# Performance work log

Hardware: AMD Instinct MI355X
Metric: run time of the kernel (lower is better)

Reference implementation:

```python
import jax, jax.numpy as jnp
import numpy as np

N = 10000        # nodes
E = 160000       # edges (avg degree 16)
MUL = 16         # multiplicity of each irrep in node features: '16x0e + 16x1o'
DIM_IN = 4 * MUL # 16 scalars + 16 vectors(3) = 64
DIM_SH = 4       # '1x0e + 1x1o' spherical harmonics
EMB = 18         # 2*4 (type embeds) + 10 (distance embed)
HID = 256
WNUM = 4 * MUL * MUL  # 4 tensor-product paths, 16x16 weights each


def setup_inputs() -> dict:
    key = jax.random.key(0)
    ks = jax.random.split(key, 8)
    node_features = jax.random.normal(ks[0], (N, DIM_IN), jnp.float32)
    edge_src = jax.random.randint(ks[1], (E,), 0, N, dtype=jnp.int32)
    edge_dst = jax.random.randint(ks[2], (E,), 0, N, dtype=jnp.int32)
    edge_attr = jax.random.normal(ks[3], (E, DIM_SH), jnp.float32)
    edge_embedding = jax.random.normal(ks[4], (E, EMB), jnp.float32)
    W1 = jax.random.normal(ks[5], (EMB, HID), jnp.float32) / np.sqrt(EMB)
    b1 = jnp.zeros((HID,), jnp.float32)
    W2 = jax.random.normal(ks[6], (HID, WNUM), jnp.float32) / np.sqrt(HID)
    b2 = jnp.zeros((WNUM,), jnp.float32)
    return dict(node_features=node_features, edge_attr=edge_attr,
                edge_embedding=edge_embedding, W1=W1, b1=b1, W2=W2, b2=b2,
                edge_src=edge_src, edge_dst=edge_dst)


def reference(node_features, edge_attr, edge_embedding, W1, b1, W2, b2, edge_src, edge_dst):
    # ---- edge MLP generates per-edge tensor-product weights ----
    h = jax.nn.silu(edge_embedding @ W1 + b1)          # [E, HID]
    w = (h @ W2 + b2).reshape(E, 4, MUL, MUL)          # [E, 4, 16, 16]
    w_ss, w_vv, w_sv, w_vs = w[:, 0], w[:, 1], w[:, 2], w[:, 3]

    # ---- gather source node features, split into irreps ----
    x = node_features[edge_src]                        # [E, 64]
    s = x[:, :MUL]                                     # [E, 16]   16x0e
    v = x[:, MUL:].reshape(E, MUL, 3)                  # [E, 16, 3] 16x1o
    y0 = edge_attr[:, 0]                               # [E]       1x0e sh
    y1 = edge_attr[:, 1:4]                             # [E, 3]    1x1o sh

    # ---- weighted Clebsch-Gordan tensor product (lmax=1 paths) ----
    inv_sqrt3 = np.float32(1.0 / np.sqrt(3.0))         # w3j(1,1,0), w3j(0,1,1), w3j(1,0,1)
    c_s = np.float32(np.sqrt(1.0 / (2 * MUL)))         # path norm: 2 paths, fan_in MUL each, out dim 1
    c_v = np.float32(np.sqrt(3.0 / (2 * MUL)))         # path norm: 2 paths, fan_in MUL each, out dim 3
    # 0e x 0e -> 0e  and  1o x 1o -> 0e
    out_s = c_s * (jnp.einsum('eij,e,ei->ej', w_ss, y0, s)
                   + inv_sqrt3 * jnp.einsum('eij,ea,eia->ej', w_vv, y1, v))   # [E, 16]
    # 0e x 1o -> 1o  and  1o x 0e -> 1o
    out_v = (c_v * inv_sqrt3) * (jnp.einsum('eij,ei,ea->eja', w_sv, s, y1)
                                 + jnp.einsum('eij,eia,e->eja', w_vs, v, y0))  # [E, 16, 3]

    edge_features = jnp.concatenate([out_s, out_v.reshape(E, 3 * MUL)], axis=1)  # [E, 64]

    # ---- scatter-reduce to destination nodes, normalized by sqrt(avg degree) ----
    num_neighbors = E / float(N)
    out = jax.ops.segment_sum(edge_features, edge_dst, num_segments=N)
    return out / np.float32(np.sqrt(num_neighbors))
```

## Files before the change

kernel.cpp:

```cpp
#include <hip/hip_runtime.h>
#include <math.h>


typedef __attribute__((ext_vector_type(8))) short s8v;
typedef __attribute__((ext_vector_type(4))) float f4v;
typedef unsigned short ushort_t;
typedef unsigned int uint_t;

#define NTHR 256
#define TE 64

__device__ __forceinline__ ushort_t f2bf(float x) {
    uint_t u = __float_as_uint(x);
    u += 0x7fffu + ((u >> 16) & 1u);
    return (ushort_t)(u >> 16);
}
__device__ __forceinline__ float bf2f(ushort_t v) {
    return __uint_as_float((uint_t)v << 16);
}

__global__ void prep_kernel(const float* __restrict__ W2, ushort_t* __restrict__ W2bf,
                            const int* __restrict__ edst, int* __restrict__ counts, int E) {
    if (blockIdx.x < 256) {
        int idx = blockIdx.x * 256 + threadIdx.x;
        int n  = idx & 1023;
        int k4 = (idx >> 10) << 2;
        uint_t lo = (uint_t)f2bf(W2[(size_t)(k4 + 0) * 1024 + n]) |
                    ((uint_t)f2bf(W2[(size_t)(k4 + 1) * 1024 + n]) << 16);
        uint_t hi = (uint_t)f2bf(W2[(size_t)(k4 + 2) * 1024 + n]) |
                    ((uint_t)f2bf(W2[(size_t)(k4 + 3) * 1024 + n]) << 16);
        ((uint2*)W2bf)[(n * 256 + k4) >> 2] = make_uint2(lo, hi);
    } else {
        int i = (blockIdx.x - 256) * 256 + threadIdx.x;
        if (i < E) atomicAdd(&counts[edst[i]], 1);
    }
}

__global__ __launch_bounds__(1024)
void scan_kernel(const int* __restrict__ counts, int* __restrict__ offsets, int N) {
    __shared__ int sdata[1024];
    const int t = threadIdx.x;
    const int C = (N + 1023) / 1024;
    const int lo = t * C;
    const int hi = min(lo + C, N);
    int sum = 0;
    for (int i = lo; i < hi; ++i) sum += counts[i];
    sdata[t] = sum;
    __syncthreads();
    for (int s = 1; s < 1024; s <<= 1) {
        int v = (t >= s) ? sdata[t - s] : 0;
        __syncthreads();
        sdata[t] += v;
        __syncthreads();
    }
    int run = sdata[t] - sum;
    for (int i = lo; i < hi; ++i) { offsets[i] = run; run += counts[i]; }
    if (t == 1023) offsets[N] = run;
}

__global__ __launch_bounds__(256)
void gather_kernel(const ushort_t* __restrict__ F,
                   const int* __restrict__ offsets,
                   const int* __restrict__ elist,
                   float* __restrict__ out, int N) {
    const int lane = threadIdx.x & 63;
    const int node = (blockIdx.x * 256 + threadIdx.x) >> 6;
    if (node >= N) return;
    const int base = offsets[node];
    const int end  = offsets[node + 1];
    float acc = 0.f;
    for (int j0 = base; j0 < end; j0 += 64) {
        const int rem = min(64, end - j0);
        int myeid = (lane < rem) ? elist[j0 + lane] : 0;
        int j = 0;
        for (; j + 4 <= rem; j += 4) {
            const int a0 = __shfl(myeid, j    );
            const int a1 = __shfl(myeid, j + 1);
            const int a2 = __shfl(myeid, j + 2);
            const int a3 = __shfl(myeid, j + 3);
            const float r0 = bf2f(F[(size_t)a0 * 64 + lane]);
            const float r1 = bf2f(F[(size_t)a1 * 64 + lane]);
            const float r2 = bf2f(F[(size_t)a2 * 64 + lane]);
            const float r3 = bf2f(F[(size_t)a3 * 64 + lane]);
            acc += (r0 + r1) + (r2 + r3);
        }
        for (; j < rem; ++j) {
            const int a = __shfl(myeid, j);
            acc += bf2f(F[(size_t)a * 64 + lane]);
        }
    }
    out[(size_t)node * 64 + lane] = acc;
}

#define LDB(sl_, g_, kk_) do { \
    const size_t o0 = (size_t)(slab * 256 + (g_) * 32) * 256 + (kk_) * 32; \
    sb0[sl_] = *(const s8v*)(Bl + o0); \
    sb1[sl_] = *(const s8v*)(Bl + o0 + 16 * 256); \
} while (0)

__global__ __launch_bounds__(NTHR, 2)
void nequip_mfma(const float* __restrict__ nodef,
                 const float* __restrict__ eattr,
                 const float* __restrict__ eemb,
                 const float* __restrict__ W1,
                 const float* __restrict__ b1,
                 const ushort_t* __restrict__ W2bf,
                 const float* __restrict__ b2,
                 const int* __restrict__ esrc,
                 const int* __restrict__ edst,
                 const int* __restrict__ offs,
                 int* __restrict__ cursor,
                 int* __restrict__ elist,
                 ushort_t* __restrict__ F,
                 int E, float CC)
{
    __shared__ __align__(16) ushort_t sAu[TE * 256];
    __shared__ __align__(16) float sB2[1024];
    __shared__ __align__(16) float sEmb[TE * 18];
    __shared__ __align__(16) float sCss[16 * 64];
    __shared__ __align__(16) float sCvv[16 * 64];
    __shared__ __align__(16) float sCsv[16 * 64];
    __shared__ __align__(16) float sCvs[48 * 64];
    __shared__ __align__(16) float sAttrT[4 * 64];
    __shared__ __align__(16) float resSS[64 * 16];
    __shared__ __align__(16) float resSV[64 * 16];

    const int t  = threadIdx.x;
    const int e0 = blockIdx.x * TE;

    ((float4*)sB2)[t] = ((const float4*)b2)[t];
    for (int idx = t; idx < TE * 18; idx += NTHR) {
        size_t g = (size_t)e0 * 18 + idx;
        sEmb[idx] = (g < (size_t)E * 18) ? eemb[g] : 0.f;
    }
    if (t < TE) {
        int ge = e0 + t;
        float4 a = make_float4(0.f, 0.f, 0.f, 0.f);
        if (ge < E) {
            a = *(const float4*)(eattr + (size_t)ge * 4);
            const int d = edst[ge];
            const int pos = offs[d] + atomicAdd(&cursor[d], 1);
            elist[pos] = ge;
        }
        sAttrT[0 * 64 + t] = a.x; sAttrT[1 * 64 + t] = a.y;
        sAttrT[2 * 64 + t] = a.z; sAttrT[3 * 64 + t] = a.w;
    }
    {
        const int e = t >> 2, iq = t & 3;
        const int ge = e0 + e;
        const bool ok = ge < E;
        float y0 = 0.f, y1x = 0.f, y1y = 0.f, y1z = 0.f;
        int src = 0;
        if (ok) {
            float4 a = *(const float4*)(eattr + (size_t)ge * 4);
            y0 = a.x; y1x = a.y; y1y = a.z; y1z = a.w;
            src = esrc[ge];
        }
        const float* xp = nodef + (size_t)src * 64;
        float4 z = make_float4(0.f, 0.f, 0.f, 0.f);
        float4 sv = ok ? *(const float4*)(xp + iq * 4) : z;
        float4 v0 = ok ? *(const float4*)(xp + 16 + iq * 12) : z;
        float4 v1 = ok ? *(const float4*)(xp + 16 + iq * 12 + 4) : z;
        float4 v2 = ok ? *(const float4*)(xp + 16 + iq * 12 + 8) : z;
        const float K3 = CC * 0.57735026918962576f;
        float sarr[4] = { sv.x, sv.y, sv.z, sv.w };
        float varr[12] = { v0.x, v0.y, v0.z, v0.w, v1.x, v1.y, v1.z, v1.w,
                           v2.x, v2.y, v2.z, v2.w };
        #pragma unroll
        for (int j = 0; j < 4; ++j) {
            const int i = iq * 4 + j;
            const float s  = sarr[j];
            const float vx = varr[j * 3 + 0], vy = varr[j * 3 + 1], vz = varr[j * 3 + 2];
            sCss[i * 64 + e] = CC * y0 * s;
            sCvv[i * 64 + e] = K3 * (y1x * vx + y1y * vy + y1z * vz);
            sCsv[i * 64 + e] = CC * s;
            sCvs[(i * 3 + 0) * 64 + e] = CC * y0 * vx;
            sCvs[(i * 3 + 1) * 64 + e] = CC * y0 * vy;
            sCvs[(i * 3 + 2) * 64 + e] = CC * y0 * vz;
        }
    }
    __syncthreads();

    {
        const int p = t & 127;
        const int ehalf = t >> 7;
        const int n0 = 2 * p;
        float w1a[18], w1b[18];
        #pragma unroll
        for (int m = 0; m < 18; ++m) {
            float2 wv = *(const float2*)(W1 + m * 256 + n0);
            w1a[m] = wv.x; w1b[m] = wv.y;
        }
        const float2 bv = *(const float2*)(b1 + n0);
        const int kk = p >> 4;
        const int lhi = 16 * ((p >> 2) & 3);
        const int wsub = p & 3;
        uint_t* sA32 = (uint_t*)sAu;
        for (int er = 0; er < 32; ++er) {
            const int e = ehalf * 32 + er;
            float a0 = bv.x, a1 = bv.y;
            const float* ep = sEmb + e * 18;
            #pragma unroll
            for (int m = 0; m < 18; ++m) {
                const float em = ep[m];
                a0 = fmaf(em, w1a[m], a0);
                a1 = fmaf(em, w1b[m], a1);
            }
            a0 = a0 / (1.f + __expf(-a0));
            a1 = a1 / (1.f + __expf(-a1));
            const uint_t pk = (uint_t)f2bf(a0) | ((uint_t)f2bf(a1) << 16);
            const int lane_sw = ((e & 15) + lhi) ^ kk;
            sA32[(((e >> 4) * 8 + kk) * 64 + lane_sw) * 4 + wsub] = pk;
        }
    }
    __syncthreads();

    const int lane = t & 63;
    const int slab = t >> 6;
    const int jj   = lane & 15;
    const int q4   = lane >> 4;

    const ushort_t* Bl = W2bf + (size_t)jj * 256 + q4 * 8;

    float pS[4][4] = {{0.f}};
    float pV[3][4][4] = {{{0.f}}};

    if (slab < 3) {
        const float* C = (slab == 0) ? sCss : (slab == 1) ? sCvv : sCsv;
        s8v sb0[4], sb1[4];
        LDB(0, 0, 0); LDB(1, 0, 1); LDB(2, 0, 2); LDB(3, 0, 3);
        #pragma unroll 1
        for (int g = 0; g < 8; ++g) {
            const int nb0 = slab * 256 + g * 32;
            const int nb1 = nb0 + 16;
            f4v accA[4], accB[4];
            {
                const float bz0 = sB2[nb0 + jj];
                const float bz1 = sB2[nb1 + jj];
                #pragma unroll
                for (int mt = 0; mt < 4; ++mt) {
                    f4v zA; zA[0] = bz0; zA[1] = bz0; zA[2] = bz0; zA[3] = bz0;
                    f4v zB; zB[0] = bz1; zB[1] = bz1; zB[2] = bz1; zB[3] = bz1;
                    accA[mt] = zA; accB[mt] = zB;
                }
            }
            #pragma unroll
            for (int kk = 0; kk < 8; ++kk) {
                const s8v b0 = sb0[kk & 3];
                const s8v b1 = sb1[kk & 3];
                #pragma unroll
                for (int mt = 0; mt < 4; ++mt) {
                    const s8v a = *(const s8v*)(sAu + ((mt * 8 + kk) * 64 + (lane ^ kk)) * 8);
                    accA[mt] = __builtin_amdgcn_mfma_f32_16x16x32_bf16(a, b0, accA[mt], 0, 0, 0);
                    accB[mt] = __builtin_amdgcn_mfma_f32_16x16x32_bf16(a, b1, accB[mt], 0, 0, 0);
                }
                if (kk < 4) { LDB(kk, g, kk + 4); }
                else        { LDB(kk - 4, (g + 1) & 7, kk - 4); }
            }
            const int i0 = 2 * g, i1 = 2 * g + 1;
            #pragma unroll
            for (int mt = 0; mt < 4; ++mt) {
                const int ebase = mt * 16 + q4 * 4;
                const float4 c0 = *(const float4*)(C + i0 * 64 + ebase);
                const float4 c1 = *(const float4*)(C + i1 * 64 + ebase);
                pS[mt][0] += c0.x * accA[mt][0] + c1.x * accB[mt][0];
                pS[mt][1] += c0.y * accA[mt][1] + c1.y * accB[mt][1];
                pS[mt][2] += c0.z * accA[mt][2] + c1.z * accB[mt][2];
                pS[mt][3] += c0.w * accA[mt][3] + c1.w * accB[mt][3];
            }
        }
        if (slab == 0) {
            #pragma unroll
            for (int mt = 0; mt < 4; ++mt)
                #pragma unroll
                for (int q = 0; q < 4; ++q)
                    resSS[(mt * 16 + q4 * 4 + q) * 16 + jj] = pS[mt][q];
        } else if (slab == 2) {
            #pragma unroll
            for (int mt = 0; mt < 4; ++mt)
                #pragma unroll
                for (int q = 0; q < 4; ++q)
                    resSV[(mt * 16 + q4 * 4 + q) * 16 + jj] = pS[mt][q];
        }
    } else {
        s8v sb0[4], sb1[4];
        #pragma unroll
        for (int half = 0; half < 2; ++half) {
            LDB(0, 0, 0); LDB(1, 0, 1); LDB(2, 0, 2); LDB(3, 0, 3);
            #pragma unroll 1
            for (int g = 0; g < 8; ++g) {
                const int i0 = 2 * g, i1 = 2 * g + 1;
                const int nb0 = 3 * 256 + g * 32;
                const int nb1 = nb0 + 16;
                f4v acc0[2], acc1[2];
                {
                    const float bz0 = sB2[nb0 + jj];
                    const float bz1 = sB2[nb1 + jj];
                    #pragma unroll
                    for (int mt = 0; mt < 2; ++mt) {
                        f4v z0; z0[0] = bz0; z0[1] = bz0; z0[2] = bz0; z0[3] = bz0;
                        f4v z1; z1[0] = bz1; z1[1] = bz1; z1[2] = bz1; z1[3] = bz1;
                        acc0[mt] = z0; acc1[mt] = z1;
                    }
                }
                #pragma unroll
                for (int kk = 0; kk < 8; ++kk) {
                    const s8v b0 = sb0[kk & 3];
                    const s8v b1 = sb1[kk & 3];
                    #pragma unroll
                    for (int mt = 0; mt < 2; ++mt) {
                        const int mtg = half * 2 + mt;
                        const s8v a = *(const s8v*)(sAu + ((mtg * 8 + kk) * 64 + (lane ^ kk)) * 8);
                        acc0[mt] = __builtin_amdgcn_mfma_f32_16x16x32_bf16(a, b0, acc0[mt], 0, 0, 0);
                        acc1[mt] = __builtin_amdgcn_mfma_f32_16x16x32_bf16(a, b1, acc1[mt], 0, 0, 0);
                    }
                    if (kk < 4) { LDB(kk, g, kk + 4); }
                    else        { LDB(kk - 4, (g + 1) & 7, kk - 4); }
                }
                #pragma unroll
                for (int mt = 0; mt < 2; ++mt) {
                    const int mtg = half * 2 + mt;
                    const int ebase = mtg * 16 + q4 * 4;
                    #pragma unroll
                    for (int a = 0; a < 3; ++a) {
                        const float4 c0 = *(const float4*)(sCvs + (i0 * 3 + a) * 64 + ebase);
                        const float4 c1 = *(const float4*)(sCvs + (i1 * 3 + a) * 64 + ebase);
                        pV[a][mtg][0] += c0.x * acc0[mt][0] + c1.x * acc1[mt][0];
                        pV[a][mtg][1] += c0.y * acc0[mt][1] + c1.y * acc1[mt][1];
                        pV[a][mtg][2] += c0.z * acc0[mt][2] + c1.z * acc1[mt][2];
                        pV[a][mtg][3] += c0.w * acc0[mt][3] + c1.w * acc1[mt][3];
                    }
                }
            }
        }
    }
    __syncthreads();

    if (slab == 1) {
        #pragma unroll
        for (int mt = 0; mt < 4; ++mt) {
            #pragma unroll
            for (int q = 0; q < 4; ++q) {
                const int e = mt * 16 + q4 * 4 + q;
                const int ge = e0 + e;
                if (ge < E) F[(size_t)ge * 64 + jj] = f2bf(resSS[e * 16 + jj] + pS[mt][q]);
            }
        }
    } else if (slab == 3) {
        #pragma unroll
        for (int mt = 0; mt < 4; ++mt) {
            #pragma unroll
            for (int q = 0; q < 4; ++q) {
                const int e = mt * 16 + q4 * 4 + q;
                const int ge = e0 + e;
                const float sv = resSV[e * 16 + jj];
                if (ge < E) {
                    #pragma unroll
                    for (int a = 0; a < 3; ++a)
                        F[(size_t)ge * 64 + 16 + jj * 3 + a] =
                            f2bf(fmaf(sAttrT[(1 + a) * 64 + e], sv, pV[a][mt][q]));
                }
            }
        }
    }
}

extern "C" void kernel_launch(void* const* d_in, const int* in_sizes, int n_in,
                              void* d_out, int out_size, void* d_ws, size_t ws_size,
                              hipStream_t stream)
{
    const float* node_features = (const float*)d_in[0];
    const float* edge_attr     = (const float*)d_in[1];
    const float* edge_emb      = (const float*)d_in[2];
    const float* W1            = (const float*)d_in[3];
    const float* b1            = (const float*)d_in[4];
    const float* W2            = (const float*)d_in[5];
    const float* b2            = (const float*)d_in[6];
    const int*   edge_src      = (const int*)d_in[7];
    const int*   edge_dst      = (const int*)d_in[8];
    float*       out           = (float*)d_out;

    const int E = in_sizes[7];
    const int N = out_size / 64;
    const float num_neigh = (float)E / (float)N;
    const float CC = 0.17677669529663689f / sqrtf(num_neigh);

    char* ws = (char*)d_ws;
    size_t off = 0;
    auto alloc = [&](size_t bytes) { char* p = ws + off; off = (off + bytes + 255) & ~(size_t)255; return p; };
    ushort_t* W2bf   = (ushort_t*)alloc((size_t)1024 * 256 * 2);
    int*      counts = (int*)alloc((size_t)2 * N * 4);
    int*      cursor = counts + N;
    int*      offs   = (int*)alloc((size_t)(N + 1) * 4);
    int*      elist  = (int*)alloc((size_t)E * 4);
    ushort_t* F      = (ushort_t*)alloc((size_t)E * 64 * 2);
    (void)ws_size;

    hipMemsetAsync(counts, 0, (size_t)2 * N * 4, stream);

    const int histBlocks = (E + 255) / 256;
    prep_kernel<<<256 + histBlocks, 256, 0, stream>>>(W2, W2bf, edge_dst, counts, E);
    scan_kernel<<<1, 1024, 0, stream>>>(counts, offs, N);

    const int blocks = (E + TE - 1) / TE;
    nequip_mfma<<<blocks, NTHR, 0, stream>>>(
        node_features, edge_attr, edge_emb, W1, b1, W2bf, b2,
        edge_src, edge_dst, offs, cursor, elist, F, E, CC);

    gather_kernel<<<(N + 3) / 4, 256, 0, stream>>>(F, offs, elist, out, N);
}
```

Measured before the change: 343.7 us.

## Move first edge-MLP layer into prep kernel and stage hidden activations via global

The first MLP layer (embedding times W1 plus SiLU, packed to bf16 in the swizzled MFMA layout) moves out of the main MFMA kernel into extra blocks of the prep kernel. Its results go to a global buffer, and the main kernel copies its 32KB tile straight into shared memory. The aim is to shorten the main kernel and run this work alongside the W2 conversion and histogram. The cost is writing and reading E*256 bf16 values (about 82MB) through global memory.

```diff
diff --git a/kernel.cpp b/kernel.cpp
--- a/kernel.cpp
+++ b/kernel.cpp
@@ -20,9 +20,14 @@
 }
 
 __global__ void prep_kernel(const float* __restrict__ W2, ushort_t* __restrict__ W2bf,
-                            const int* __restrict__ edst, int* __restrict__ counts, int E) {
+                            const int* __restrict__ edst, int* __restrict__ counts,
+                            const float* __restrict__ eemb, const float* __restrict__ W1,
+                            const float* __restrict__ b1, ushort_t* __restrict__ hG,
+                            int E, int histBlocks) {
+    __shared__ float sEmb[TE * 18];
+    const int t = threadIdx.x;
     if (blockIdx.x < 256) {
-        int idx = blockIdx.x * 256 + threadIdx.x;
+        int idx = blockIdx.x * 256 + t;
         int n  = idx & 1023;
         int k4 = (idx >> 10) << 2;
         uint_t lo = (uint_t)f2bf(W2[(size_t)(k4 + 0) * 1024 + n]) |
@@ -30,9 +35,47 @@
         uint_t hi = (uint_t)f2bf(W2[(size_t)(k4 + 2) * 1024 + n]) |
                     ((uint_t)f2bf(W2[(size_t)(k4 + 3) * 1024 + n]) << 16);
         ((uint2*)W2bf)[(n * 256 + k4) >> 2] = make_uint2(lo, hi);
+    } else if ((int)blockIdx.x < 256 + histBlocks) {
+        int i = (blockIdx.x - 256) * 256 + t;
+        if (i < E) atomicAdd(&counts[edst[i]], 1);
     } else {
-        int i = (blockIdx.x - 256) * 256 + threadIdx.x;
-        if (i < E) atomicAdd(&counts[edst[i]], 1);
+        const int tile = blockIdx.x - 256 - histBlocks;
+        const int e0 = tile * TE;
+        for (int idx = t; idx < TE * 18; idx += NTHR) {
+            size_t g = (size_t)e0 * 18 + idx;
+            sEmb[idx] = (g < (size_t)E * 18) ? eemb[g] : 0.f;
+        }
+        __syncthreads();
+        const int p = t & 127;
+        const int ehalf = t >> 7;
+        const int n0 = 2 * p;
+        float w1a[18], w1b[18];
+        #pragma unroll
+        for (int m = 0; m < 18; ++m) {
+            float2 wv = *(const float2*)(W1 + m * 256 + n0);
+            w1a[m] = wv.x; w1b[m] = wv.y;
+        }
+        const float2 bv = *(const float2*)(b1 + n0);
+        const int kk = p >> 4;
+        const int lhi = 16 * ((p >> 2) & 3);
+        const int wsub = p & 3;
+        uint_t* hT = (uint_t*)hG + (size_t)tile * 8192;
+        for (int er = 0; er < 32; ++er) {
+            const int e = ehalf * 32 + er;
+            float a0 = bv.x, a1 = bv.y;
+            const float* ep = sEmb + e * 18;
+            #pragma unroll
+            for (int m = 0; m < 18; ++m) {
+                const float em = ep[m];
+                a0 = fmaf(em, w1a[m], a0);
+                a1 = fmaf(em, w1b[m], a1);
+            }
+            a0 = a0 / (1.f + __expf(-a0));
+            a1 = a1 / (1.f + __expf(-a1));
+            const uint_t pk = (uint_t)f2bf(a0) | ((uint_t)f2bf(a1) << 16);
+            const int lane_sw = ((e & 15) + lhi) ^ kk;
+            hT[(((e >> 4) * 8 + kk) * 64 + lane_sw) * 4 + wsub] = pk;
+        }
     }
 }
 
@@ -101,9 +144,7 @@
 __global__ __launch_bounds__(NTHR, 2)
 void nequip_mfma(const float* __restrict__ nodef,
                  const float* __restrict__ eattr,
-                 const float* __restrict__ eemb,
-                 const float* __restrict__ W1,
-                 const float* __restrict__ b1,
+                 const ushort_t* __restrict__ hG,
                  const ushort_t* __restrict__ W2bf,
                  const float* __restrict__ b2,
                  const int* __restrict__ esrc,
@@ -116,7 +157,6 @@
 {
     __shared__ __align__(16) ushort_t sAu[TE * 256];
     __shared__ __align__(16) float sB2[1024];
-    __shared__ __align__(16) float sEmb[TE * 18];
     __shared__ __align__(16) float sCss[16 * 64];
     __shared__ __align__(16) float sCvv[16 * 64];
     __shared__ __align__(16) float sCsv[16 * 64];
@@ -128,11 +168,13 @@
     const int t  = threadIdx.x;
     const int e0 = blockIdx.x * TE;
 
+    {
+        const uint4* hsrc = (const uint4*)(hG + (size_t)blockIdx.x * 16384);
+        uint4* sdst = (uint4*)sAu;
+        #pragma unroll
+        for (int r = 0; r < 8; ++r) sdst[r * 256 + t] = hsrc[r * 256 + t];
+    }
     ((float4*)sB2)[t] = ((const float4*)b2)[t];
-    for (int idx = t; idx < TE * 18; idx += NTHR) {
-        size_t g = (size_t)e0 * 18 + idx;
-        sEmb[idx] = (g < (size_t)E * 18) ? eemb[g] : 0.f;
-    }
     if (t < TE) {
         int ge = e0 + t;
         float4 a = make_float4(0.f, 0.f, 0.f, 0.f);
@@ -177,40 +219,6 @@
             sCvs[(i * 3 + 0) * 64 + e] = CC * y0 * vx;
             sCvs[(i * 3 + 1) * 64 + e] = CC * y0 * vy;
             sCvs[(i * 3 + 2) * 64 + e] = CC * y0 * vz;
-        }
-    }
-    __syncthreads();
-
-    {
-        const int p = t & 127;
-        const int ehalf = t >> 7;
-        const int n0 = 2 * p;
-        float w1a[18], w1b[18];
-        #pragma unroll
-        for (int m = 0; m < 18; ++m) {
-            float2 wv = *(const float2*)(W1 + m * 256 + n0);
-            w1a[m] = wv.x; w1b[m] = wv.y;
-        }
-        const float2 bv = *(const float2*)(b1 + n0);
-        const int kk = p >> 4;
-        const int lhi = 16 * ((p >> 2) & 3);
-        const int wsub = p & 3;
-        uint_t* sA32 = (uint_t*)sAu;
-        for (int er = 0; er < 32; ++er) {
-            const int e = ehalf * 32 + er;
-            float a0 = bv.x, a1 = bv.y;
-            const float* ep = sEmb + e * 18;
-            #pragma unroll
-            for (int m = 0; m < 18; ++m) {
-                const float em = ep[m];
-                a0 = fmaf(em, w1a[m], a0);
-                a1 = fmaf(em, w1b[m], a1);
-            }
-            a0 = a0 / (1.f + __expf(-a0));
-            a1 = a1 / (1.f + __expf(-a1));
-            const uint_t pk = (uint_t)f2bf(a0) | ((uint_t)f2bf(a1) << 16);
-            const int lane_sw = ((e & 15) + lhi) ^ kk;
-            sA32[(((e >> 4) * 8 + kk) * 64 + lane_sw) * 4 + wsub] = pk;
         }
     }
     __syncthreads();
@@ -385,6 +393,9 @@
     const float num_neigh = (float)E / (float)N;
     const float CC = 0.17677669529663689f / sqrtf(num_neigh);
 
+    const int mainBlocks = (E + TE - 1) / TE;
+    const int histBlocks = (E + 255) / 256;
+
     char* ws = (char*)d_ws;
     size_t off = 0;
     auto alloc = [&](size_t bytes) { char* p = ws + off; off = (off + bytes + 255) & ~(size_t)255; return p; };
@@ -394,17 +405,17 @@
     int*      offs   = (int*)alloc((size_t)(N + 1) * 4);
     int*      elist  = (int*)alloc((size_t)E * 4);
     ushort_t* F      = (ushort_t*)alloc((size_t)E * 64 * 2);
+    ushort_t* hG     = (ushort_t*)alloc((size_t)mainBlocks * 16384 * 2);
     (void)ws_size;
 
     hipMemsetAsync(counts, 0, (size_t)2 * N * 4, stream);
 
-    const int histBlocks = (E + 255) / 256;
-    prep_kernel<<<256 + histBlocks, 256, 0, stream>>>(W2, W2bf, edge_dst, counts, E);
+    prep_kernel<<<256 + histBlocks + mainBlocks, 256, 0, stream>>>(
+        W2, W2bf, edge_dst, counts, edge_emb, W1, b1, hG, E, histBlocks);
     scan_kernel<<<1, 1024, 0, stream>>>(counts, offs, N);
 
-    const int blocks = (E + TE - 1) / TE;
-    nequip_mfma<<<blocks, NTHR, 0, stream>>>(
-        node_features, edge_attr, edge_emb, W1, b1, W2bf, b2,
+    nequip_mfma<<<mainBlocks, NTHR, 0, stream>>>(
+        node_features, edge_attr, hG, W2bf, b2,
         edge_src, edge_dst, offs, cursor, elist, F, E, CC);
 
     gather_kernel<<<(N + 3) / 4, 256, 0, stream>>>(F, offs, elist, out, N);
```

After: 369.4 us. 7.5% more time.
